# Kernel optimization log

Measured on AMD Instinct MI355X. Metric: run time of the kernel, lower is better.

## Reference

```python
import jax, jax.numpy as jnp
import numpy as np

IN_DIM = 64
OUT_DIM = 128
GROUPS = 4
KS = 3
PAD = 1
SPLINE_ORDER = 3
GRID_SIZE = 5
GRID_K = GRID_SIZE + SPLINE_ORDER  # 8
GRID_LO, GRID_HI = -1.0, 1.0
_H = (GRID_HI - GRID_LO) / GRID_SIZE
GRID = jnp.linspace(GRID_LO - _H * SPLINE_ORDER, GRID_HI + _H * SPLINE_ORDER,
                    GRID_SIZE + 2 * SPLINE_ORDER + 1, dtype=jnp.float32)  # [14]
EPS = 1e-5


def _conv(x, w):
    # NCHW x OIHW -> NCHW, stride 1, dilation 1, padding PAD
    return jax.lax.conv_general_dilated(
        x, w, window_strides=(1, 1), padding=((PAD, PAD), (PAD, PAD)),
        dimension_numbers=('NCHW', 'OIHW', 'NCHW'))


def _bspline_bases(x):
    # Cox-de-Boor recursion; x: [B,C,H,W] -> [B, C*GRID_K, H, W]
    xu = x[..., None]  # [B,C,H,W,1]
    g = GRID
    bases = ((xu >= g[:-1]) & (xu < g[1:])).astype(x.dtype)  # [B,C,H,W,13]
    for k in range(1, SPLINE_ORDER + 1):
        left = g[:-(k + 1)]
        right = g[k:-1]
        delta = jnp.where(right == left, jnp.ones_like(right), right - left)
        bases = ((xu - left) / delta * bases[..., :-1]
                 + (g[k + 1:] - xu) / (g[k + 1:] - g[1:-k]) * bases[..., 1:])
    B, C, H, W, K = bases.shape  # K == GRID_K
    # moveaxis(-1, 2) then flatten(1, 2): channel-major, basis-minor ordering
    return jnp.moveaxis(bases, -1, 2).reshape(B, C * K, H, W)


def setup_inputs() -> dict:
    key = jax.random.key(0)
    k1, k2 = jax.random.split(key)
    x = jax.random.normal(k1, (8, IN_DIM, 64, 64), dtype=jnp.float32)
    # layer_weight: [out/g, (in/g)*(grid_k+1), ks, ks] = [32, 144, 3, 3]
    layer_weight = jax.random.normal(
        k2, (OUT_DIM // GROUPS, (IN_DIM // GROUPS) * (GRID_K + 1), KS, KS),
        dtype=jnp.float32) * 0.05
    prelu_w = jnp.full((GROUPS,), 0.25, dtype=jnp.float32)  # torch PReLU init
    return {"x": x, "layer_weight": layer_weight, "prelu_w": prelu_w}


def reference(x, layer_weight, prelu_w):
    cin_g = IN_DIM // GROUPS
    cout_g = OUT_DIM // GROUPS
    base_w = layer_weight[:, -cin_g:].reshape(cout_g, cin_g, KS, KS)
    spline_w = layer_weight[:, :-cin_g].reshape(cout_g, cin_g * GRID_K, KS, KS)
    outs = []
    for g in range(GROUPS):
        xg = x[:, g * cin_g:(g + 1) * cin_g]
        base_out = _conv(jax.nn.gelu(xg, approximate=False), base_w)
        spline_out = _conv(_bspline_bases(xg), spline_w)
        y = base_out + spline_out
        # InstanceNorm2d (affine=False): per-sample per-channel spatial norm
        mu = y.mean(axis=(2, 3), keepdims=True)
        var = y.var(axis=(2, 3), keepdims=True)
        y = (y - mu) / jnp.sqrt(var + EPS)
        # PReLU with scalar slope per group
        y = jnp.where(y >= 0, y, prelu_w[g] * y)
        outs.append(y)
    return jnp.concatenate(outs, axis=1)  # [B, OUT_DIM, H, W]
```

## Files before the change

kernel.cpp:

```cpp
#include <hip/hip_runtime.h>
#include <hip/hip_bf16.h>
#include <math.h>

typedef __attribute__((ext_vector_type(8))) short short8;
typedef __attribute__((ext_vector_type(4))) float f32x4;
typedef __attribute__((ext_vector_type(16))) float f32x16;
typedef unsigned int u32;
typedef unsigned long long u64;

__global__ void wtrans(const float* __restrict__ lw, ushort* __restrict__ w2) {
    int t = blockIdx.x * 256 + threadIdx.x;
    if (t >= 5184) return;
    int l    = t & 63;
    int page = t >> 6;
    int ks  = page % 9;
    int tap = page / 9;
    int oc = l & 31;
    int kbase = ks * 16 + ((l >> 5) << 3);
    short8 v;
#pragma unroll
    for (int e = 0; e < 8; ++e) {
        int k = kbase + e;
        float val = lw[(oc * 144 + k) * 9 + tap];
        __hip_bfloat16 hb = __float2bfloat16(val);
        v[e] = *(short*)&hb;
    }
    ((short8*)w2)[t] = v;
}

__global__ __launch_bounds__(256) void kanconv(const float* __restrict__ x,
                                               const ushort* __restrict__ w2,
                                               float* __restrict__ y) {
    __shared__ __align__(16) ushort Fs[108 * 152];
    const int tid  = threadIdx.x;
    const int tile = blockIdx.x;
    const int b    = blockIdx.y;
    const int g    = blockIdx.z;
    const int h0 = (tile >> 2) * 4;
    const int w0 = (tile & 3) * 16;
    const float* xg = x + ((size_t)(b * 64 + g * 16)) * 4096;

#pragma unroll 1
    for (int it = 0; it < 7; ++it) {
        int e = it * 256 + tid;
        if (e < 1728) {
            int icg = e / 108;
            int p   = e - icg * 108;
            int py = p / 18, px = p - py * 18;
            int hy = h0 + py - 1, wx = w0 + px - 1;
            bool img = ((unsigned)hy < 64u) && ((unsigned)wx < 64u);
            float xv = img ? xg[icg * 4096 + hy * 64 + wx] : 0.f;
            float tpos = (xv + 2.2f) * 2.5f;
            float cf = floorf(tpos);
            int ci = (int)cf;
            float u = tpos - cf;
            float u2 = u * u, u3 = u2 * u, om = 1.f - u;
            const float s6 = 1.f / 6.f;
            float q0 = om * om * om * s6;
            float q1 = (4.f - 6.f * u2 + 3.f * u3) * s6;
            float q2 = (1.f + 3.f * u + 3.f * u2 - 3.f * u3) * s6;
            float q3 = u3 * s6;
            __hip_bfloat16 hq0 = __float2bfloat16(q0);
            __hip_bfloat16 hq1 = __float2bfloat16(q1);
            __hip_bfloat16 hq2 = __float2bfloat16(q2);
            __hip_bfloat16 hq3 = __float2bfloat16(q3);
            u64 Q =   (u64)*(ushort*)&hq0
                    | ((u64)*(ushort*)&hq1 << 16)
                    | ((u64)*(ushort*)&hq2 << 32)
                    | ((u64)*(ushort*)&hq3 << 48);
            u64 lo = 0, hi = 0;
            if (img && ci >= 0 && ci <= 10) {
                int s = ci * 16 - 48;
                if (s < 0)        { lo = Q >> (-s); }
                else if (s < 64)  { lo = Q << s; hi = s ? (Q >> (64 - s)) : 0ull; }
                else              { hi = Q << (s - 64); }
            }
            union { u64 u64v[2]; short8 s8; } un;
            un.u64v[0] = lo; un.u64v[1] = hi;
            ushort* row = &Fs[p * 152];
            *(short8*)(row + icg * 8) = un.s8;
            float z  = xv * 0.70710678118654752f;
            float az = fabsf(z);
            float tt = 1.f / fmaf(0.3275911f, az, 1.f);
            float poly = tt * fmaf(tt, fmaf(tt, fmaf(tt, fmaf(tt, 1.061405429f,
                          -1.453152027f), 1.421413741f), -0.284496736f),
                          0.254829592f);
            float er = 1.f - poly * __expf(-z * z);
            er = (z < 0.f) ? -er : er;
            float ge = 0.5f * xv * (1.f + er);
            __hip_bfloat16 hg = __float2bfloat16(ge);
            row[128 + icg] = *(ushort*)&hg;
        }
    }
    __syncthreads();

    const int wv = tid >> 6;
    const int l  = tid & 63;
    const int khalf = wv & 1;
    const int pt    = wv >> 1;
    const int pix  = pt * 32 + (l & 31);
    const int prow = pix >> 4, pcol = pix & 15;
    const int klo  = l >> 5;

    f32x16 acc;
#pragma unroll
    for (int i = 0; i < 16; ++i) acc[i] = 0.f;
    const short8* w8 = (const short8*)w2;
    const int tap_lo = khalf ? 5 : 0;
    const int tap_hi = khalf ? 9 : 5;

#pragma unroll 1
    for (int tap = tap_lo; tap < tap_hi; ++tap) {
        const int kh = tap / 3, kw = tap - kh * 3;
        const ushort* fb = &Fs[((prow + kh) * 18 + (pcol + kw)) * 152 + klo * 8];
        const short8* ap = w8 + tap * 576 + l;
#pragma unroll
        for (int ks = 0; ks < 9; ++ks) {
            short8 a  = ap[ks * 64];
            short8 bf = *(const short8*)(fb + ks * 16);
            acc = __builtin_amdgcn_mfma_f32_32x32x16_bf16(a, bf, acc, 0, 0, 0);
        }
    }

    __syncthreads();
    float* comb = (float*)Fs;
    if (khalf == 1) {
        float* cp = comb + (pt * 64 + l) * 20;
        *(f32x4*)(cp + 0)  = f32x4{acc[0], acc[1], acc[2], acc[3]};
        *(f32x4*)(cp + 4)  = f32x4{acc[4], acc[5], acc[6], acc[7]};
        *(f32x4*)(cp + 8)  = f32x4{acc[8], acc[9], acc[10], acc[11]};
        *(f32x4*)(cp + 12) = f32x4{acc[12], acc[13], acc[14], acc[15]};
    }
    __syncthreads();
    if (khalf == 0) {
        const float* cp = comb + (pt * 64 + l) * 20;
        float* yb = y + (((size_t)b * 128 + g * 32) * 64 + h0 + prow) * 64
                      + w0 + pcol;
#pragma unroll
        for (int r = 0; r < 16; ++r) {
            int oc = (r & 3) + 8 * (r >> 2) + 4 * klo;
            yb[(size_t)oc * 4096] = acc[r] + cp[r];
        }
    }
}

__global__ __launch_bounds__(256) void instnorm(float* __restrict__ y,
                                                const float* __restrict__ prelu) {
    const int blk = blockIdx.x;
    const int tid = threadIdx.x;
    float4* yp = (float4*)(y + (size_t)blk * 4096);
    float4 v0 = yp[tid], v1 = yp[tid + 256], v2 = yp[tid + 512], v3 = yp[tid + 768];
    float s  = v0.x + v0.y + v0.z + v0.w + v1.x + v1.y + v1.z + v1.w
             + v2.x + v2.y + v2.z + v2.w + v3.x + v3.y + v3.z + v3.w;
    float s2 = v0.x*v0.x + v0.y*v0.y + v0.z*v0.z + v0.w*v0.w
             + v1.x*v1.x + v1.y*v1.y + v1.z*v1.z + v1.w*v1.w
             + v2.x*v2.x + v2.y*v2.y + v2.z*v2.z + v2.w*v2.w
             + v3.x*v3.x + v3.y*v3.y + v3.z*v3.z + v3.w*v3.w;
#pragma unroll
    for (int off = 32; off > 0; off >>= 1) {
        s  += __shfl_down(s, off);
        s2 += __shfl_down(s2, off);
    }
    __shared__ float red[8];
    int wave = tid >> 6;
    if ((tid & 63) == 0) { red[wave] = s; red[4 + wave] = s2; }
    __syncthreads();
    float S  = red[0] + red[1] + red[2] + red[3];
    float S2 = red[4] + red[5] + red[6] + red[7];
    float mean = S * (1.0f / 4096.0f);
    float var  = S2 * (1.0f / 4096.0f) - mean * mean;
    float rstd = rsqrtf(var + 1e-5f);
    float slope = prelu[(blk >> 5) & 3];
    float t;
    float4 o;
#define NRM(vv)                                                               \
    t = (vv.x - mean) * rstd; o.x = t >= 0.f ? t : slope * t;                 \
    t = (vv.y - mean) * rstd; o.y = t >= 0.f ? t : slope * t;                 \
    t = (vv.z - mean) * rstd; o.z = t >= 0.f ? t : slope * t;                 \
    t = (vv.w - mean) * rstd; o.w = t >= 0.f ? t : slope * t;
    NRM(v0); yp[tid]       = o;
    NRM(v1); yp[tid + 256] = o;
    NRM(v2); yp[tid + 512] = o;
    NRM(v3); yp[tid + 768] = o;
#undef NRM
}

extern "C" void kernel_launch(void* const* d_in, const int* in_sizes, int n_in,
                              void* d_out, int out_size, void* d_ws, size_t ws_size,
                              hipStream_t stream) {
    const float* x     = (const float*)d_in[0];
    const float* lw    = (const float*)d_in[1];
    const float* prelu = (const float*)d_in[2];
    float*  out = (float*)d_out;
    ushort* w2  = (ushort*)d_ws;

    wtrans<<<21, 256, 0, stream>>>(lw, w2);
    dim3 grid(64, 8, 4);
    kanconv<<<grid, 256, 0, stream>>>(x, w2, out);
    instnorm<<<1024, 256, 0, stream>>>(out, prelu);
}
```

Baseline: 42.68 us.

## Split conv taps across four waves, reuse weight fragments, batch input loads

Each wave now covers both 32-pixel halves of the tile and a subset of the nine taps. A single weight fragment load therefore feeds two MFMAs, roughly halving weight traffic per MFMA. The four partial sums are reduced through shared memory in the epilogue. Input loads for the feature build are also hoisted into a separate unrolled loop to raise memory-level parallelism, and launch bounds request four blocks per SM. The costs are two accumulators per wave, a heavier cross-wave reduction, and an uneven tap split (wave 3 gets three taps).

```diff
diff --git a/kernel.cpp b/kernel.cpp
--- a/kernel.cpp
+++ b/kernel.cpp
@@ -28,9 +28,9 @@
     ((short8*)w2)[t] = v;
 }
 
-__global__ __launch_bounds__(256) void kanconv(const float* __restrict__ x,
-                                               const ushort* __restrict__ w2,
-                                               float* __restrict__ y) {
+__global__ __launch_bounds__(256, 4) void kanconv(const float* __restrict__ x,
+                                                  const ushort* __restrict__ w2,
+                                                  float* __restrict__ y) {
     __shared__ __align__(16) ushort Fs[108 * 152];
     const int tid  = threadIdx.x;
     const int tile = blockIdx.x;
@@ -40,17 +40,34 @@
     const int w0 = (tile & 3) * 16;
     const float* xg = x + ((size_t)(b * 64 + g * 16)) * 4096;
 
-#pragma unroll 1
+    float xv[7];
+    unsigned imgbits = 0;
+#pragma unroll
+    for (int it = 0; it < 7; ++it) {
+        int e = it * 256 + tid;
+        float v = 0.f;
+        if (e < 1728) {
+            int icg = e / 108;
+            int p   = e - icg * 108;
+            int py = p / 18, px = p - py * 18;
+            int hy = h0 + py - 1, wx = w0 + px - 1;
+            if (((unsigned)hy < 64u) && ((unsigned)wx < 64u)) {
+                v = xg[icg * 4096 + hy * 64 + wx];
+                imgbits |= (1u << it);
+            }
+        }
+        xv[it] = v;
+    }
+
+#pragma unroll
     for (int it = 0; it < 7; ++it) {
         int e = it * 256 + tid;
         if (e < 1728) {
             int icg = e / 108;
             int p   = e - icg * 108;
-            int py = p / 18, px = p - py * 18;
-            int hy = h0 + py - 1, wx = w0 + px - 1;
-            bool img = ((unsigned)hy < 64u) && ((unsigned)wx < 64u);
-            float xv = img ? xg[icg * 4096 + hy * 64 + wx] : 0.f;
-            float tpos = (xv + 2.2f) * 2.5f;
+            bool img = (imgbits >> it) & 1u;
+            float v = xv[it];
+            float tpos = (v + 2.2f) * 2.5f;
             float cf = floorf(tpos);
             int ci = (int)cf;
             float u = tpos - cf;
@@ -79,7 +96,7 @@
             un.u64v[0] = lo; un.u64v[1] = hi;
             ushort* row = &Fs[p * 152];
             *(short8*)(row + icg * 8) = un.s8;
-            float z  = xv * 0.70710678118654752f;
+            float z  = v * 0.70710678118654752f;
             float az = fabsf(z);
             float tt = 1.f / fmaf(0.3275911f, az, 1.f);
             float poly = tt * fmaf(tt, fmaf(tt, fmaf(tt, fmaf(tt, 1.061405429f,
@@ -87,7 +104,7 @@
                           0.254829592f);
             float er = 1.f - poly * __expf(-z * z);
             er = (z < 0.f) ? -er : er;
-            float ge = 0.5f * xv * (1.f + er);
+            float ge = 0.5f * v * (1.f + er);
             __hip_bfloat16 hg = __float2bfloat16(ge);
             row[128 + icg] = *(ushort*)&hg;
         }
@@ -96,50 +113,75 @@
 
     const int wv = tid >> 6;
     const int l  = tid & 63;
-    const int khalf = wv & 1;
-    const int pt    = wv >> 1;
-    const int pix  = pt * 32 + (l & 31);
-    const int prow = pix >> 4, pcol = pix & 15;
-    const int klo  = l >> 5;
-
-    f32x16 acc;
-#pragma unroll
-    for (int i = 0; i < 16; ++i) acc[i] = 0.f;
+    const int la = l & 31, klo = l >> 5;
+    const int p0row = la >> 4, p0col = la & 15;
+
+    f32x16 accA, accB;
+#pragma unroll
+    for (int i = 0; i < 16; ++i) { accA[i] = 0.f; accB[i] = 0.f; }
     const short8* w8 = (const short8*)w2;
-    const int tap_lo = khalf ? 5 : 0;
-    const int tap_hi = khalf ? 9 : 5;
+    const int tap_lo = wv * 2;
+    const int tap_hi = (wv == 3) ? 9 : wv * 2 + 2;
 
 #pragma unroll 1
     for (int tap = tap_lo; tap < tap_hi; ++tap) {
         const int kh = tap / 3, kw = tap - kh * 3;
-        const ushort* fb = &Fs[((prow + kh) * 18 + (pcol + kw)) * 152 + klo * 8];
+        const ushort* fb0 = &Fs[((p0row + kh) * 18 + (p0col + kw)) * 152 + klo * 8];
+        const ushort* fb1 = fb0 + 2 * 18 * 152;
         const short8* ap = w8 + tap * 576 + l;
 #pragma unroll
         for (int ks = 0; ks < 9; ++ks) {
-            short8 a  = ap[ks * 64];
-            short8 bf = *(const short8*)(fb + ks * 16);
-            acc = __builtin_amdgcn_mfma_f32_32x32x16_bf16(a, bf, acc, 0, 0, 0);
+            short8 a   = ap[ks * 64];
+            short8 bf0 = *(const short8*)(fb0 + ks * 16);
+            short8 bf1 = *(const short8*)(fb1 + ks * 16);
+            accA = __builtin_amdgcn_mfma_f32_32x32x16_bf16(a, bf0, accA, 0, 0, 0);
+            accB = __builtin_amdgcn_mfma_f32_32x32x16_bf16(a, bf1, accB, 0, 0, 0);
         }
     }
 
     __syncthreads();
     float* comb = (float*)Fs;
-    if (khalf == 1) {
-        float* cp = comb + (pt * 64 + l) * 20;
-        *(f32x4*)(cp + 0)  = f32x4{acc[0], acc[1], acc[2], acc[3]};
-        *(f32x4*)(cp + 4)  = f32x4{acc[4], acc[5], acc[6], acc[7]};
-        *(f32x4*)(cp + 8)  = f32x4{acc[8], acc[9], acc[10], acc[11]};
-        *(f32x4*)(cp + 12) = f32x4{acc[12], acc[13], acc[14], acc[15]};
-    }
-    __syncthreads();
-    if (khalf == 0) {
-        const float* cp = comb + (pt * 64 + l) * 20;
+    if (wv != 0) {
+        float* cp = comb + ((wv * 2 + 0) * 64 + l) * 16;
+        *(f32x4*)(cp + 0)  = f32x4{accA[0], accA[1], accA[2], accA[3]};
+        *(f32x4*)(cp + 4)  = f32x4{accA[4], accA[5], accA[6], accA[7]};
+        *(f32x4*)(cp + 8)  = f32x4{accA[8], accA[9], accA[10], accA[11]};
+        *(f32x4*)(cp + 12) = f32x4{accA[12], accA[13], accA[14], accA[15]};
+    }
+    if (wv != 1) {
+        float* cp = comb + ((wv * 2 + 1) * 64 + l) * 16;
+        *(f32x4*)(cp + 0)  = f32x4{accB[0], accB[1], accB[2], accB[3]};
+        *(f32x4*)(cp + 4)  = f32x4{accB[4], accB[5], accB[6], accB[7]};
+        *(f32x4*)(cp + 8)  = f32x4{accB[8], accB[9], accB[10], accB[11]};
+        *(f32x4*)(cp + 12) = f32x4{accB[12], accB[13], accB[14], accB[15]};
+    }
+    __syncthreads();
+    if (wv < 2) {
+        f32x16 sum = (wv == 0) ? accA : accB;
+#pragma unroll
+        for (int w = 0; w < 4; ++w) {
+            if (w == wv) continue;
+            const float* cp = comb + ((w * 2 + wv) * 64 + l) * 16;
+            f32x4 c0 = *(const f32x4*)(cp + 0);
+            f32x4 c1 = *(const f32x4*)(cp + 4);
+            f32x4 c2 = *(const f32x4*)(cp + 8);
+            f32x4 c3 = *(const f32x4*)(cp + 12);
+#pragma unroll
+            for (int r = 0; r < 4; ++r) {
+                sum[r]      += c0[r];
+                sum[r + 4]  += c1[r];
+                sum[r + 8]  += c2[r];
+                sum[r + 12] += c3[r];
+            }
+        }
+        const int pix = wv * 32 + la;
+        const int prow = pix >> 4, pcol = pix & 15;
         float* yb = y + (((size_t)b * 128 + g * 32) * 64 + h0 + prow) * 64
                       + w0 + pcol;
 #pragma unroll
         for (int r = 0; r < 16; ++r) {
             int oc = (r & 3) + 8 * (r >> 2) + 4 * klo;
-            yb[(size_t)oc * 4096] = acc[r] + cp[r];
+            yb[(size_t)oc * 4096] = sum[r];
         }
     }
 }
```

New measurement: 40.78 us. 1.05x faster.
